# Optimization experiments

Hardware: AMD Instinct MI355X
Metric: run time of the kernel (lower is better)

## Reference

```python
import math
import jax, jax.numpy as jnp
import numpy as np

NH, D, MULT, VOCAB, NLAYER = 4, 256, 128, 256, 2
N = MULT * D // NH  # 8192
EPS = 1e-5
THETA = 2.0 ** 16


def get_freqs(n):
    q = (jnp.arange(n, dtype=jnp.float32) // 2) * 2  # quantize(t, 2)
    return 1.0 / (THETA ** (q / n)) / (2 * math.pi)


def ln(x):
    # LayerNorm over last dim, no affine
    mu = jnp.mean(x, axis=-1, keepdims=True)
    var = jnp.mean((x - mu) ** 2, axis=-1, keepdims=True)
    return (x - mu) / jnp.sqrt(var + EPS)


def rope(phases, v):
    # phases: (T, N), v: (B, nh, T, N)
    ph = (phases % 1.0) * (2 * math.pi)
    c, s = jnp.cos(ph), jnp.sin(ph)
    v_rot = jnp.stack((-v[..., 1::2], v[..., ::2]), axis=-1).reshape(v.shape)
    return v * c + v_rot * s


def setup_inputs() -> dict:
    key = jax.random.key(0)
    ks = jax.random.split(key, 6)
    std = 0.02
    return {
        "idx": jax.random.randint(ks[0], (1, 2048), 0, VOCAB),
        "embed": jax.random.normal(ks[1], (VOCAB, D), jnp.float32) * std,
        "encoder": jax.random.normal(ks[2], (NH, D, N), jnp.float32) * std,
        "encoder_v": jax.random.normal(ks[3], (NH, D, N), jnp.float32) * std,
        "decoder": jax.random.normal(ks[4], (NH * N, D), jnp.float32) * std,
        "lm_head": jax.random.normal(ks[5], (D, VOCAB), jnp.float32) * std,
    }


def reference(idx, embed, encoder, encoder_v, decoder, lm_head):
    B, T = idx.shape
    freqs = get_freqs(N)  # (N,)
    phases = jnp.arange(T, dtype=jnp.float32)[:, None] * freqs[None, :]  # (T, N)
    # strictly-lower-triangular causal mask (tril diagonal=-1)
    t = jnp.arange(T)
    mask = (t[:, None] > t[None, :]).astype(jnp.float32)  # (T, T)

    x = ln(embed[idx][:, None])  # (B, 1, T, D)
    for _ in range(NLAYER):
        x_sparse = jax.nn.relu(jnp.einsum('bltd,hdn->bhtn', x, encoder))  # (B,nh,T,N)
        QR = rope(phases, x_sparse)
        scores = jnp.einsum('bhtn,bhsn->bhts', QR, QR) * mask  # (B,nh,T,T)
        yKV = ln(jnp.einsum('bhts,blsd->bhtd', scores, x))  # (B,nh,T,D)
        y_sparse = jax.nn.relu(jnp.einsum('bhtd,hdn->bhtn', yKV, encoder_v))
        xy = x_sparse * y_sparse  # (B,nh,T,N)
        xy = xy.transpose(0, 2, 1, 3).reshape(B, 1, T, NH * N)
        yMLP = xy @ decoder  # (B,1,T,D)
        x = ln(x + ln(yMLP))
    logits = x[:, 0] @ lm_head  # (B,T,vocab)
    return logits
```

## Files before the change

### kernel.cpp

```cpp
#include <hip/hip_runtime.h>
#include <hip/hip_bf16.h>
#include <math.h>

typedef unsigned short u16;
typedef unsigned int u32;
typedef __attribute__((ext_vector_type(8))) short short8;
typedef __attribute__((ext_vector_type(4))) float f32x4;

__device__ __forceinline__ u16 f2b(float f) {
  u32 u = __builtin_bit_cast(u32, f);
  u = (u + 0x7fffu + ((u >> 16) & 1u)) >> 16;
  return (u16)u;
}
__device__ __forceinline__ float b2f(u16 s) {
  return __builtin_bit_cast(float, (u32)s << 16);
}

__device__ __forceinline__ void ld_g2l(const u16* g, u16* l) {
  __builtin_amdgcn_global_load_lds(
      (const __attribute__((address_space(1))) unsigned int*)g,
      (__attribute__((address_space(3))) unsigned int*)l, 16, 0, 0);
}

__device__ __forceinline__ void gemm_core64(
    const u16* __restrict__ A, const u16* __restrict__ B,
    int lda, int ldb, int Klen, int kb, int bm, int bn,
    u16* __restrict__ A0, u16* __restrict__ A1,
    u16* __restrict__ B0, u16* __restrict__ B1, f32x4 (&acc)[4][4])
{
  int tid = threadIdx.x;
  int w = tid >> 6, lane = tid & 63;
  int srow = (w << 4) + (lane >> 2);
  int scol = (lane & 3) << 3;
  const u16* ga0 = A + (long)(bm * 128 + srow) * lda + kb + scol;
  const u16* ga1 = ga0 + (long)64 * lda;
  const u16* gb0 = B + (long)(bn * 128 + srow) * ldb + kb + scol;
  const u16* gb1 = gb0 + (long)64 * ldb;
  int lo = w << 9;

  int wm = (w >> 1) << 6, wn = (w & 1) << 6;
  int lane15 = lane & 15, quad = lane >> 4;
  int fro = (wm + lane15) * 32 + quad * 8;
  int fco = (wn + lane15) * 32 + quad * 8;

#pragma unroll
  for (int i = 0; i < 4; i++)
#pragma unroll
    for (int j = 0; j < 4; j++) { f32x4 z = {0.f, 0.f, 0.f, 0.f}; acc[i][j] = z; }

  for (int k = 0; k < Klen; k += 64) {
    ld_g2l(ga0 + k,      A0 + lo); ld_g2l(ga1 + k,      A0 + lo + 2048);
    ld_g2l(ga0 + k + 32, A1 + lo); ld_g2l(ga1 + k + 32, A1 + lo + 2048);
    ld_g2l(gb0 + k,      B0 + lo); ld_g2l(gb1 + k,      B0 + lo + 2048);
    ld_g2l(gb0 + k + 32, B1 + lo); ld_g2l(gb1 + k + 32, B1 + lo + 2048);
    __syncthreads();
#pragma unroll
    for (int kg = 0; kg < 2; kg++) {
      const u16* ar = (kg ? A1 : A0) + fro;
      const u16* br = (kg ? B1 : B0) + fco;
      short8 af[4], bfr[4];
#pragma unroll
      for (int mt = 0; mt < 4; mt++) af[mt] = *(const short8*)(ar + mt * 512);
#pragma unroll
      for (int nt = 0; nt < 4; nt++) bfr[nt] = *(const short8*)(br + nt * 512);
#pragma unroll
      for (int mt = 0; mt < 4; mt++)
#pragma unroll
        for (int nt = 0; nt < 4; nt++)
          acc[mt][nt] = __builtin_amdgcn_mfma_f32_16x16x32_bf16(af[mt], bfr[nt], acc[mt][nt], 0, 0, 0);
    }
    __syncthreads();
  }
}

template<int EPI>
__global__ __launch_bounds__(256, 2) void gemm_bt(
    const u16* __restrict__ A, const u16* __restrict__ B, void* __restrict__ C,
    int K, int lda, int ldb, int ldc, int nsplits, long aB, long bB, long cB,
    int tri)
{
  __shared__ __align__(16) u16 A0[4096], A1[4096], B0[4096], B1[4096];
  int bn = blockIdx.x, bm = blockIdx.y;
  int batch = blockIdx.z / nsplits, sp = blockIdx.z % nsplits;
  int Klen = K / nsplits, kb = sp * Klen;
  if (tri) {
    int kend = (bm + 1) * 128;
    if (kb >= kend) return;
    if (kb + Klen > kend) Klen = kend - kb;
  }

  f32x4 acc[4][4];
  gemm_core64(A + (long)batch * aB, B + (long)batch * bB, lda, ldb, Klen, kb,
              bm, bn, A0, A1, B0, B1, acc);

  int lane = threadIdx.x & 63, w = threadIdx.x >> 6;
  int wm = (w >> 1) << 6, wn = (w & 1) << 6;
  int lane15 = lane & 15, quad = lane >> 4;

  if (EPI == 1 || EPI == 4) {
    u16* Cp = (u16*)C;
#pragma unroll
    for (int nt = 0; nt < 4; nt++) {
      int gn = bn * 128 + wn + nt * 16 + lane15;
      float f = exp2f((float)(-(gn & ~1)) * (1.0f / 512.0f)) * 0.15915494f;
      int t0 = bm * 128 + wm + quad * 4;
      float ph0 = (float)t0 * f; ph0 -= floorf(ph0);
      float s0, c0; __sincosf(ph0 * 6.2831853f, &s0, &c0);
      float s1, c1; __sincosf(f * 6.2831853f, &s1, &c1);
      float ph16 = 16.f * f; ph16 -= floorf(ph16);
      float s16, c16; __sincosf(ph16 * 6.2831853f, &s16, &c16);
      float cm = c0, sm = s0;
#pragma unroll
      for (int mt = 0; mt < 4; mt++) {
        float cr = cm, sr = sm;
#pragma unroll
        for (int r = 0; r < 4; r++) {
          int gm = bm * 128 + wm + mt * 16 + quad * 4 + r;
          float v = acc[mt][nt][r];
          long ci = (long)batch * cB + (long)gm * ldc + gn;
          if (EPI == 1) {
            float rv = fmaxf(v, 0.f);
            float ro = __shfl_xor(rv, 1);
            float out = (gn & 1) ? (rv * cr + ro * sr) : (rv * cr - ro * sr);
            Cp[ci] = f2b(out);
          } else {
            float qv = b2f(Cp[ci]);
            float qo = __shfl_xor(qv, 1);
            float xs = (gn & 1) ? (qv * cr - qo * sr) : (qv * cr + qo * sr);
            Cp[ci] = f2b(fmaxf(v, 0.f) * xs);
          }
          float cn = cr * c1 - sr * s1; sr = sr * c1 + cr * s1; cr = cn;
        }
        float cn2 = cm * c16 - sm * s16; sm = sm * c16 + cm * s16; cm = cn2;
      }
    }
  } else {
#pragma unroll
    for (int mt = 0; mt < 4; mt++)
#pragma unroll
      for (int nt = 0; nt < 4; nt++) {
        int gn = bn * 128 + wn + nt * 16 + lane15;
#pragma unroll
        for (int r = 0; r < 4; r++) {
          int gm = bm * 128 + wm + mt * 16 + quad * 4 + r;
          float v = acc[mt][nt][r];
          long ci = (long)batch * cB + (long)gm * ldc + gn;
          if (EPI == 0) ((float*)C)[ci] = v;
          else          atomicAdd(&((float*)C)[ci], v);
        }
      }
  }
}

__global__ __launch_bounds__(256, 2) void gemm_scores(
    const u16* __restrict__ QR, u16* __restrict__ S, int T)
{
  __shared__ __align__(16) u16 A0[4096], A1[4096], B0[4096], B1[4096];
  int t = blockIdx.x;
  int bm = (int)((sqrtf(8.0f * t + 1.0f) - 1.0f) * 0.5f);
  while ((bm + 1) * (bm + 2) / 2 <= t) bm++;
  while (bm * (bm + 1) / 2 > t) bm--;
  int bn = t - bm * (bm + 1) / 2;

  const u16* Q = QR + (long)blockIdx.y * (long)T * 8192;
  u16* Sb = S + (long)blockIdx.y * (long)T * T;

  f32x4 acc[4][4];
  gemm_core64(Q, Q, 8192, 8192, 8192, 0, bm, bn, A0, A1, B0, B1, acc);

  int lane = threadIdx.x & 63, w = threadIdx.x >> 6;
  int wm = (w >> 1) << 6, wn = (w & 1) << 6;
  int lane15 = lane & 15, quad = lane >> 4;
#pragma unroll
  for (int mt = 0; mt < 4; mt++)
#pragma unroll
    for (int nt = 0; nt < 4; nt++)
#pragma unroll
      for (int r = 0; r < 4; r++) {
        int gm = bm * 128 + wm + mt * 16 + quad * 4 + r;
        int gn = bn * 128 + wn + nt * 16 + lane15;
        Sb[(long)gm * T + gn] = f2b(gm > gn ? acc[mt][nt][r] : 0.f);
      }
}

__global__ __launch_bounds__(256) void trans_f32_bf16(
    const float* __restrict__ src, u16* __restrict__ dst, int R, int C)
{
  __shared__ float tile[32][33];
  long off = (long)blockIdx.z * R * C;
  const float* s = src + off;
  u16* d = dst + off;
  int lx = threadIdx.x & 31, ly = threadIdx.x >> 5;
  int c = blockIdx.x * 32 + lx;
#pragma unroll
  for (int p = 0; p < 32; p += 8)
    tile[ly + p][lx] = s[(long)(blockIdx.y * 32 + ly + p) * C + c];
  __syncthreads();
  int rr = blockIdx.y * 32 + lx;
#pragma unroll
  for (int p = 0; p < 32; p += 8)
    d[(long)(blockIdx.x * 32 + ly + p) * R + rr] = f2b(tile[lx][ly + p]);
}

__device__ __forceinline__ float block_sum(float v, float* red) {
#pragma unroll
  for (int o = 32; o > 0; o >>= 1) v += __shfl_down(v, o, 64);
  int lane = threadIdx.x & 63, wid = threadIdx.x >> 6;
  if (lane == 0) red[wid] = v;
  __syncthreads();
  float r = red[0] + red[1] + red[2] + red[3];
  __syncthreads();
  return r;
}

__global__ __launch_bounds__(256) void embed_ln(
    const int* __restrict__ idx, const float* __restrict__ embed,
    float* __restrict__ x, u16* __restrict__ xb, u16* __restrict__ xT, int T)
{
  __shared__ float red[4];
  int t = blockIdx.x, d = threadIdx.x;
  float v = embed[(long)idx[t] * 256 + d];
  float mu = block_sum(v, red) * (1.f / 256.f);
  float c = v - mu;
  float var = block_sum(c * c, red) * (1.f / 256.f);
  float o = c * rsqrtf(var + 1e-5f);
  x[(long)t * 256 + d] = o;
  xb[(long)t * 256 + d] = f2b(o);
  xT[(long)d * T + t] = f2b(o);
}

__global__ __launch_bounds__(256) void row_ln(
    const float* __restrict__ in, u16* __restrict__ out)
{
  __shared__ float red[4];
  long row = blockIdx.x;
  int d = threadIdx.x;
  float v = in[row * 256 + d];
  float mu = block_sum(v, red) * (1.f / 256.f);
  float c = v - mu;
  float var = block_sum(c * c, red) * (1.f / 256.f);
  out[row * 256 + d] = f2b(c * rsqrtf(var + 1e-5f));
}

__global__ __launch_bounds__(256) void resid_ln(
    const float* __restrict__ yMLP, float* __restrict__ x,
    u16* __restrict__ xb, u16* __restrict__ xT, int T)
{
  __shared__ float red[4];
  int t = blockIdx.x, d = threadIdx.x;
  float y = yMLP[(long)t * 256 + d];
  float mu1 = block_sum(y, red) * (1.f / 256.f);
  float c1 = y - mu1;
  float var1 = block_sum(c1 * c1, red) * (1.f / 256.f);
  float l1 = c1 * rsqrtf(var1 + 1e-5f);
  float v = x[(long)t * 256 + d] + l1;
  float mu2 = block_sum(v, red) * (1.f / 256.f);
  float c2 = v - mu2;
  float var2 = block_sum(c2 * c2, red) * (1.f / 256.f);
  float o = c2 * rsqrtf(var2 + 1e-5f);
  x[(long)t * 256 + d] = o;
  xb[(long)t * 256 + d] = f2b(o);
  xT[(long)d * T + t] = f2b(o);
}

extern "C" void kernel_launch(void* const* d_in, const int* in_sizes, int n_in,
                              void* d_out, int out_size, void* d_ws, size_t ws_size,
                              hipStream_t stream) {
  const int*   idx       = (const int*)d_in[0];
  const float* embed     = (const float*)d_in[1];
  const float* encoder   = (const float*)d_in[2];
  const float* encoder_v = (const float*)d_in[3];
  const float* decoder   = (const float*)d_in[4];
  const float* lm_head   = (const float*)d_in[5];
  const int T = in_sizes[0];
  const int D = 256, NH = 4, Nn = 8192, V = 256;
  const int TB = T / 128, ntri = TB * (TB + 1) / 2;

  char* ws = (char*)d_ws;
  size_t off = 0;
  auto alloc = [&](size_t bytes) -> void* {
    void* p = ws + off; off += (bytes + 255) & ~(size_t)255; return p;
  };
  float* x_f32   = (float*)alloc((size_t)T * D * 4);
  float* yMLP    = (float*)alloc((size_t)T * D * 4);
  float* yKV_f32 = (float*)alloc((size_t)NH * T * D * 4);
  u16* x_b    = (u16*)alloc((size_t)T * D * 2);
  u16* xT     = (u16*)alloc((size_t)T * D * 2);
  u16* yKV_b  = (u16*)alloc((size_t)NH * T * D * 2);
  u16* lmT    = (u16*)alloc((size_t)D * V * 2);
  u16* encT   = (u16*)alloc((size_t)NH * Nn * D * 2);
  u16* encvT  = (u16*)alloc((size_t)NH * Nn * D * 2);
  u16* decT   = (u16*)alloc((size_t)D * NH * Nn * 2);
  size_t per_head = ((size_t)T * T * 2 + 256) + ((size_t)T * Nn * 2 + 256);
  int HB = 4;
  while (HB > 1 && off + (size_t)HB * per_head > ws_size) HB >>= 1;
  u16* scores = (u16*)alloc((size_t)HB * T * T * 2);
  u16* QRxy   = (u16*)alloc((size_t)HB * T * Nn * 2);
  if (off > ws_size) return;

  trans_f32_bf16<<<dim3(Nn / 32, D / 32, NH), 256, 0, stream>>>(encoder, encT, D, Nn);
  trans_f32_bf16<<<dim3(Nn / 32, D / 32, NH), 256, 0, stream>>>(encoder_v, encvT, D, Nn);
  trans_f32_bf16<<<dim3(D / 32, (NH * Nn) / 32, 1), 256, 0, stream>>>(decoder, decT, NH * Nn, D);
  trans_f32_bf16<<<dim3(V / 32, D / 32, 1), 256, 0, stream>>>(lm_head, lmT, D, V);

  embed_ln<<<T, 256, 0, stream>>>(idx, embed, x_f32, x_b, xT, T);

  for (int l = 0; l < 2; l++) {
    hipMemsetAsync(yMLP, 0, (size_t)T * D * 4, stream);
    for (int h0 = 0; h0 < NH; h0 += HB) {
      gemm_bt<1><<<dim3(Nn / 128, T / 128, HB), 256, 0, stream>>>(
          x_b, encT + (size_t)h0 * Nn * D, QRxy,
          D, D, D, Nn, 1, 0L, (long)Nn * D, (long)T * Nn, 0);
      gemm_scores<<<dim3(ntri, HB, 1), 256, 0, stream>>>(QRxy, scores, T);
      hipMemsetAsync(yKV_f32, 0, (size_t)HB * T * D * 4, stream);
      gemm_bt<3><<<dim3(D / 128, T / 128, HB * 8), 256, 0, stream>>>(
          scores, xT, yKV_f32,
          T, T, T, D, 8, (long)T * T, 0L, (long)T * D, 1);
      row_ln<<<HB * T, 256, 0, stream>>>(yKV_f32, yKV_b);
      gemm_bt<4><<<dim3(Nn / 128, T / 128, HB), 256, 0, stream>>>(
          yKV_b, encvT + (size_t)h0 * Nn * D, QRxy,
          D, D, D, Nn, 1, (long)T * D, (long)Nn * D, (long)T * Nn, 0);
      gemm_bt<3><<<dim3(D / 128, T / 128, HB * 8), 256, 0, stream>>>(
          QRxy, decT + (size_t)h0 * Nn, yMLP,
          Nn, Nn, NH * Nn, D, 8, (long)T * Nn, (long)Nn, 0L, 0);
    }
    resid_ln<<<T, 256, 0, stream>>>(yMLP, x_f32, x_b, xT, T);
  }

  gemm_bt<0><<<dim3(V / 128, T / 128, 1), 256, 0, stream>>>(
      x_b, lmT, d_out, D, D, D, V, 1, 0L, 0L, 0L, 0);
}
```

Measured before the change: 1.314 ms.

## Split-K the causal scores GEMM and reduce partials in a separate kernel

The QR·QRᵀ scores GEMM now splits its 8192-long K dimension into SK chunks, so the grid has ntri×HB×SK blocks instead of ntri×HB. Each chunk writes its bf16 partial tile to its own slice, and a new scores_cvt kernel sums the slices, applies the strict causal mask and writes the result in place to slice 0. The aim is to put more blocks in flight, since the triangular grid alone (136 tiles per head) may underfill the GPU. In exchange it adds an extra launch, extra partial-buffer traffic, and rounds each partial to bf16 before summing, which adds some precision loss.

```diff
diff --git a/kernel.cpp b/kernel.cpp
--- a/kernel.cpp
+++ b/kernel.cpp
@@ -71,6 +71,13 @@
     }
     __syncthreads();
   }
+}
+
+__device__ __forceinline__ void tri_decode(int t, int& bm, int& bn) {
+  bm = (int)((sqrtf(8.0f * t + 1.0f) - 1.0f) * 0.5f);
+  while ((bm + 1) * (bm + 2) / 2 <= t) bm++;
+  while (bm * (bm + 1) / 2 > t) bm--;
+  bn = t - bm * (bm + 1) / 2;
 }
 
 template<int EPI>
@@ -152,22 +159,19 @@
   }
 }
 
-__global__ __launch_bounds__(256, 2) void gemm_scores(
-    const u16* __restrict__ QR, u16* __restrict__ S, int T)
+__global__ __launch_bounds__(256, 2) void gemm_scores_sk(
+    const u16* __restrict__ QR, u16* __restrict__ P, int T, int SK)
 {
   __shared__ __align__(16) u16 A0[4096], A1[4096], B0[4096], B1[4096];
-  int t = blockIdx.x;
-  int bm = (int)((sqrtf(8.0f * t + 1.0f) - 1.0f) * 0.5f);
-  while ((bm + 1) * (bm + 2) / 2 <= t) bm++;
-  while (bm * (bm + 1) / 2 > t) bm--;
-  int bn = t - bm * (bm + 1) / 2;
-
-  const u16* Q = QR + (long)blockIdx.y * (long)T * 8192;
-  u16* Sb = S + (long)blockIdx.y * (long)T * T;
+  int bm, bn; tri_decode(blockIdx.x, bm, bn);
+  int h = blockIdx.y, sk = blockIdx.z;
+  const u16* Q = QR + (long)h * (long)T * 8192;
+  int Klen = 8192 / SK, kb = sk * Klen;
 
   f32x4 acc[4][4];
-  gemm_core64(Q, Q, 8192, 8192, 8192, 0, bm, bn, A0, A1, B0, B1, acc);
-
+  gemm_core64(Q, Q, 8192, 8192, Klen, kb, bm, bn, A0, A1, B0, B1, acc);
+
+  u16* Pb = P + ((long)sk * gridDim.y + h) * (long)T * T;
   int lane = threadIdx.x & 63, w = threadIdx.x >> 6;
   int wm = (w >> 1) << 6, wn = (w & 1) << 6;
   int lane15 = lane & 15, quad = lane >> 4;
@@ -179,8 +183,41 @@
       for (int r = 0; r < 4; r++) {
         int gm = bm * 128 + wm + mt * 16 + quad * 4 + r;
         int gn = bn * 128 + wn + nt * 16 + lane15;
-        Sb[(long)gm * T + gn] = f2b(gm > gn ? acc[mt][nt][r] : 0.f);
+        Pb[(long)gm * T + gn] = f2b(acc[mt][nt][r]);
       }
+}
+
+__global__ __launch_bounds__(256) void scores_cvt(
+    u16* __restrict__ P, int T, int SK, int HB)
+{
+  int bm, bn; tri_decode(blockIdx.x, bm, bn);
+  long slice = (long)HB * T * T;
+  u16* base = P + (long)blockIdx.y * (long)T * T;
+  for (int i = threadIdx.x; i < 2048; i += 256) {
+    int r = i >> 4, c8 = (i & 15) << 3;
+    int gm = bm * 128 + r, gn0 = bn * 128 + c8;
+    long o = (long)gm * T + gn0;
+    float s[8];
+#pragma unroll
+    for (int e = 0; e < 8; e++) s[e] = 0.f;
+    for (int p = 0; p < SK; p++) {
+      uint4 v = *(const uint4*)(base + p * slice + o);
+      u32 vv[4] = {v.x, v.y, v.z, v.w};
+#pragma unroll
+      for (int e = 0; e < 4; e++) {
+        s[2 * e]     += b2f((u16)(vv[e] & 0xffffu));
+        s[2 * e + 1] += b2f((u16)(vv[e] >> 16));
+      }
+    }
+    u32 out[4];
+#pragma unroll
+    for (int e = 0; e < 4; e++) {
+      float e0 = (gm > gn0 + 2 * e)     ? s[2 * e]     : 0.f;
+      float e1 = (gm > gn0 + 2 * e + 1) ? s[2 * e + 1] : 0.f;
+      out[e] = (u32)f2b(e0) | ((u32)f2b(e1) << 16);
+    }
+    *(uint4*)(base + o) = make_uint4(out[0], out[1], out[2], out[3]);
+  }
 }
 
 __global__ __launch_bounds__(256) void trans_f32_bf16(
@@ -291,11 +328,14 @@
   u16* encT   = (u16*)alloc((size_t)NH * Nn * D * 2);
   u16* encvT  = (u16*)alloc((size_t)NH * Nn * D * 2);
   u16* decT   = (u16*)alloc((size_t)D * NH * Nn * 2);
-  size_t per_head = ((size_t)T * T * 2 + 256) + ((size_t)T * Nn * 2 + 256);
+  size_t part_b = (size_t)8 * T * T * 2;
   int HB = 4;
-  while (HB > 1 && off + (size_t)HB * per_head > ws_size) HB >>= 1;
-  u16* scores = (u16*)alloc((size_t)HB * T * T * 2);
-  u16* QRxy   = (u16*)alloc((size_t)HB * T * Nn * 2);
+  while (HB > 1 &&
+         off + part_b + 256 + (size_t)HB * ((size_t)T * Nn * 2 + 256) > ws_size)
+    HB >>= 1;
+  int SK = 8 / HB;
+  u16* scoresP = (u16*)alloc(part_b);
+  u16* QRxy    = (u16*)alloc((size_t)HB * T * Nn * 2);
   if (off > ws_size) return;
 
   trans_f32_bf16<<<dim3(Nn / 32, D / 32, NH), 256, 0, stream>>>(encoder, encT, D, Nn);
@@ -311,10 +351,11 @@
       gemm_bt<1><<<dim3(Nn / 128, T / 128, HB), 256, 0, stream>>>(
           x_b, encT + (size_t)h0 * Nn * D, QRxy,
           D, D, D, Nn, 1, 0L, (long)Nn * D, (long)T * Nn, 0);
-      gemm_scores<<<dim3(ntri, HB, 1), 256, 0, stream>>>(QRxy, scores, T);
+      gemm_scores_sk<<<dim3(ntri, HB, SK), 256, 0, stream>>>(QRxy, scoresP, T, SK);
+      scores_cvt<<<dim3(ntri, HB), 256, 0, stream>>>(scoresP, T, SK, HB);
       hipMemsetAsync(yKV_f32, 0, (size_t)HB * T * D * 4, stream);
       gemm_bt<3><<<dim3(D / 128, T / 128, HB * 8), 256, 0, stream>>>(
-          scores, xT, yKV_f32,
+          scoresP, xT, yKV_f32,
           T, T, T, D, 8, (long)T * T, 0L, (long)T * D, 1);
       row_ln<<<HB * T, 256, 0, stream>>>(yKV_f32, yKV_b);
       gemm_bt<4><<<dim3(Nn / 128, T / 128, HB), 256, 0, stream>>>(
```

Result: slower. 1.396 ms (+6.3%).
